# Kernel optimization log

Hardware: AMD Instinct MI355X
Metric: run time of the kernel (lower is better)

Reference implementation:

```python
import jax, jax.numpy as jnp
import numpy as np

B, P, T = 64, 196, 30
E, D, A, ENC, V = 512, 512, 512, 512, 30000


def setup_inputs() -> dict:
    key = jax.random.key(0)
    ks = jax.random.split(key, 24)
    s = 0.02
    return {
        "encoder_feats": jax.random.normal(ks[0], (B, P, ENC), jnp.float32),
        "encoder_pooled": jax.random.normal(ks[1], (B, ENC), jnp.float32),
        "captions": jax.random.randint(ks[2], (B, T), 0, V),
        "We_att": jax.random.normal(ks[3], (ENC, A), jnp.float32) * s,
        "be_att": jnp.zeros((A,), jnp.float32),
        "Wd_att": jax.random.normal(ks[4], (D, A), jnp.float32) * s,
        "bd_att": jnp.zeros((A,), jnp.float32),
        "wf_att": jax.random.normal(ks[5], (A, 1), jnp.float32) * s,
        "bf_att": jnp.zeros((), jnp.float32),
        "emb_table": jax.random.normal(ks[6], (V, E), jnp.float32) * s,
        "W_ih": jax.random.normal(ks[7], (E + ENC, 4 * D), jnp.float32) * s,
        "W_hh": jax.random.normal(ks[8], (D, 4 * D), jnp.float32) * s,
        "b_ih": jnp.zeros((4 * D,), jnp.float32),
        "b_hh": jnp.zeros((4 * D,), jnp.float32),
        "W_init_h": jax.random.normal(ks[9], (ENC, D), jnp.float32) * s,
        "b_init_h": jnp.zeros((D,), jnp.float32),
        "W_init_c": jax.random.normal(ks[10], (ENC, D), jnp.float32) * s,
        "b_init_c": jnp.zeros((D,), jnp.float32),
        "W_fc": jax.random.normal(ks[11], (D, V), jnp.float32) * s,
        "b_fc": jnp.zeros((V,), jnp.float32),
        "W_beta": jax.random.normal(ks[12], (D, ENC), jnp.float32) * s,
        "b_beta": jnp.zeros((ENC,), jnp.float32),
    }


def reference(encoder_feats, encoder_pooled, captions, We_att, be_att, Wd_att,
              bd_att, wf_att, bf_att, emb_table, W_ih, W_hh, b_ih, b_hh,
              W_init_h, b_init_h, W_init_c, b_init_c, W_fc, b_fc, W_beta, b_beta):
    # teacher_forcing_ratio = 1.0, dropout in eval mode (identity)
    emb = emb_table[captions]                              # (B, T, E)
    h = jnp.tanh(encoder_pooled @ W_init_h + b_init_h)     # (B, D)
    c = jnp.tanh(encoder_pooled @ W_init_c + b_init_c)
    enc_proj = encoder_feats @ We_att + be_att             # (B, P, A) precomputed

    def step(carry, emb_t):
        h, c = carry
        dec_proj = h @ Wd_att + bd_att                     # (B, A)
        e = jnp.tanh(enc_proj + dec_proj[:, None, :])      # (B, P, A)
        scores = jnp.squeeze(e @ wf_att, -1) + bf_att      # (B, P)
        alpha = jax.nn.softmax(scores, axis=1)
        ctx = jnp.einsum('bp,bpd->bd', alpha, encoder_feats)
        gate = jax.nn.sigmoid(h @ W_beta + b_beta)
        ctx = gate * ctx
        x = jnp.concatenate([emb_t, ctx], axis=1)          # (B, E+ENC)
        gates = x @ W_ih + b_ih + h @ W_hh + b_hh          # (B, 4D) torch order i,f,g,o
        i, f, g, o = jnp.split(gates, 4, axis=1)
        c2 = jax.nn.sigmoid(f) * c + jax.nn.sigmoid(i) * jnp.tanh(g)
        h2 = jax.nn.sigmoid(o) * jnp.tanh(c2)
        out = h2 @ W_fc + b_fc                             # (B, V)
        return (h2, c2), out

    # inputs at steps t=1..T-1 are teacher-forced embeddings[:, t-1]
    xs = jnp.swapaxes(emb[:, :-1, :], 0, 1)                # (T-1, B, E)
    _, outs = jax.lax.scan(step, (h, c), xs)               # (T-1, B, V)
    outs = jnp.swapaxes(outs, 0, 1)                        # (B, T-1, V)
    zero0 = jnp.zeros((outs.shape[0], 1, outs.shape[2]), outs.dtype)
    return jnp.concatenate([zero0, outs], axis=1)          # (B, T, V)
```

## Files before the change

### kernel.cpp

```cpp
#include <hip/hip_runtime.h>
#include <hip/hip_bf16.h>

#define BB 64
#define PP 196
#define TT 30
#define DD 512
#define VV 30000
#define VPAD 30080
#define MROWS 1856
#define MPAD 1920
#define NBLK 64
#define ASTR 3072
#define ABUF ((size_t)64 * ASTR)

typedef __attribute__((ext_vector_type(8))) short short8;
typedef __attribute__((ext_vector_type(4))) float f32x4;

__device__ __forceinline__ unsigned short f2bf(float f) {
    unsigned int u = __float_as_uint(f);
    unsigned int r = u + 0x7FFFu + ((u >> 16) & 1u);
    return (unsigned short)(r >> 16);
}
__device__ __forceinline__ float bf2f(unsigned short u) {
    return __uint_as_float(((unsigned int)u) << 16);
}
__device__ __forceinline__ float sigf(float x) { return 1.f / (1.f + __expf(-x)); }
__device__ __forceinline__ float tanh_fast(float x) { return 1.f - 2.f / (1.f + __expf(2.f * x)); }
__device__ __forceinline__ unsigned int pack2(unsigned short a, unsigned short b) {
    return (unsigned int)a | ((unsigned int)b << 16);
}
__device__ __forceinline__ void ast_u32(unsigned int* p, unsigned int v) {
    __hip_atomic_store(p, v, __ATOMIC_RELAXED, __HIP_MEMORY_SCOPE_AGENT);
}
__device__ __forceinline__ void ast_f32(float* p, float v) {
    __hip_atomic_store(p, v, __ATOMIC_RELAXED, __HIP_MEMORY_SCOPE_AGENT);
}

__global__ __launch_bounds__(256) void k_cast(const float* __restrict__ in,
                                              unsigned short* __restrict__ out, int n) {
    int i = blockIdx.x * 256 + threadIdx.x;
    int stride = gridDim.x * 256;
    for (; i < n; i += stride) out[i] = f2bf(in[i]);
}

__global__ __launch_bounds__(256) void k_transpose_cast(const float* __restrict__ in,
                                                        unsigned short* __restrict__ out,
                                                        int R, int C, int Cpad, int ostride, int ooff) {
    __shared__ float tile[32][33];
    int tx = threadIdx.x & 31, ty = threadIdx.x >> 5;
    int c0 = blockIdx.x * 32, r0 = blockIdx.y * 32;
#pragma unroll
    for (int i = 0; i < 4; ++i) {
        int r = r0 + ty + i * 8, c = c0 + tx;
        tile[ty + i * 8][tx] = (c < C) ? in[(size_t)r * C + c] : 0.f;
    }
    __syncthreads();
#pragma unroll
    for (int i = 0; i < 4; ++i) {
        int outr = c0 + ty + i * 8, outc = r0 + tx;
        if (outr < Cpad) out[(size_t)outr * ostride + ooff + outc] = f2bf(tile[tx][ty + i * 8]);
    }
}

__global__ __launch_bounds__(256) void k_transpose_cast_split(const float* __restrict__ in,
                                                              unsigned short* __restrict__ out,
                                                              int R, int C, int ostride,
                                                              int ooff, int looff) {
    __shared__ float tile[32][33];
    int tx = threadIdx.x & 31, ty = threadIdx.x >> 5;
    int c0 = blockIdx.x * 32, r0 = blockIdx.y * 32;
#pragma unroll
    for (int i = 0; i < 4; ++i) {
        int r = r0 + ty + i * 8, c = c0 + tx;
        tile[ty + i * 8][tx] = in[(size_t)r * C + c];
    }
    __syncthreads();
#pragma unroll
    for (int i = 0; i < 4; ++i) {
        int outr = c0 + ty + i * 8, outc = r0 + tx;
        float v = tile[tx][ty + i * 8];
        unsigned short hi = f2bf(v);
        unsigned short lo = f2bf(v - bf2f(hi));
        out[(size_t)outr * ostride + ooff + outc] = hi;
        out[(size_t)outr * ostride + looff + outc] = lo;
    }
}

__global__ __launch_bounds__(256) void k_zero0(float* __restrict__ out) {
    int i = blockIdx.x * 256 + threadIdx.x;
    int b = i / VV, v = i - b * VV;
    out[(size_t)b * (TT * VV) + v] = 0.f;
}

__global__ __launch_bounds__(256) void k_init(const float* __restrict__ pooled,
                                              const float* __restrict__ Wh, const float* __restrict__ bh,
                                              const float* __restrict__ Wc, const float* __restrict__ bc,
                                              unsigned short* __restrict__ A1,
                                              float* __restrict__ cbuf, int* __restrict__ bar) {
    int b = blockIdx.x >> 1, which = blockIdx.x & 1, t = threadIdx.x;
    if (blockIdx.x == 0) {
        for (int i = t; i < NBLK * 32 + 32; i += 256) bar[i] = 0;
    }
    const float* W = which ? Wc : Wh;
    const float* bias = which ? bc : bh;
    const float* pr = pooled + b * DD;
    float a0 = 0.f, a1 = 0.f;
#pragma unroll 4
    for (int k = 0; k < DD; ++k) {
        float pv = pr[k];
        a0 += pv * W[k * DD + t];
        a1 += pv * W[k * DD + t + 256];
    }
    float v0 = tanh_fast(a0 + bias[t]);
    float v1 = tanh_fast(a1 + bias[t + 256]);
    if (which == 0) {
        unsigned short hi0 = f2bf(v0), lo0 = f2bf(v0 - bf2f(hi0));
        unsigned short hi1 = f2bf(v1), lo1 = f2bf(v1 - bf2f(hi1));
        unsigned short* xr = A1 + b * ASTR;
        xr[1024 + t] = hi0;        xr[2560 + t] = lo0;
        xr[1024 + t + 256] = hi1;  xr[2560 + t + 256] = lo1;
    } else {
        cbuf[b * DD + t] = v0;
        cbuf[b * DD + t + 256] = v1;
    }
}

__device__ __forceinline__ void gbar(int* bar, int g) {
    __syncthreads();
    asm volatile("s_waitcnt vmcnt(0)" ::: "memory");
    if (threadIdx.x == 0)
        __hip_atomic_store(&bar[blockIdx.x * 32], g, __ATOMIC_RELAXED, __HIP_MEMORY_SCOPE_AGENT);
    if (threadIdx.x < NBLK) {
        while (__hip_atomic_load(&bar[threadIdx.x * 32], __ATOMIC_RELAXED, __HIP_MEMORY_SCOPE_AGENT) < g)
            __builtin_amdgcn_s_sleep(1);
    }
    __syncthreads();
}

#define PA_SUB(S, PH, PL, TILE, NEXT)                                                          \
    ((uint4*)Sa[S])[t] = PH;                                                                   \
    ((uint4*)Sl[S])[t] = PL;                                                                   \
    { int kn = (NEXT) * 32; PH = *(const uint4*)(Ah + kn); PL = *(const uint4*)(Al + kn); }    \
    asm volatile("s_waitcnt lgkmcnt(0)" ::: "memory");                                         \
    __builtin_amdgcn_sched_barrier(0);                                                         \
    __builtin_amdgcn_s_barrier();                                                              \
    __builtin_amdgcn_sched_barrier(0);                                                         \
    { int k0 = (TILE) * 32;                                                                    \
      short8 ah = *(const short8*)&Sa[S][((wave * 16 + r16) * 4 + swz) * 8];                   \
      short8 al = *(const short8*)&Sl[S][((wave * 16 + r16) * 4 + swz) * 8];                   \
      int cu = (k0 >> 3) + kg;                                                                 \
      short8 bh = *(const short8*)&Bp_s[r16 * 1024 + ((cu ^ (r16 & 7)) << 3)];                 \
      short8 bl = *(const short8*)&Bp_s[r16 * 1024 + (((cu + 64) ^ (r16 & 7)) << 3)];          \
      acc = __builtin_amdgcn_mfma_f32_16x16x32_bf16(ah, bh, acc, 0, 0, 0);                     \
      acc = __builtin_amdgcn_mfma_f32_16x16x32_bf16(al, bh, acc, 0, 0, 0);                     \
      acc = __builtin_amdgcn_mfma_f32_16x16x32_bf16(ah, bl, acc, 0, 0, 0); }

#define PC_SUB(S, RAH, RAL, RBH, RBL, TILE, NEXT)                                              \
    ((uint4*)Sa[S])[t] = RAH;  ((uint4*)Sl[S])[t] = RAL;                                       \
    ((uint4*)Sb[S])[t] = RBH;  ((uint4*)Sbl[S])[t] = RBL;                                      \
    { int kn = (NEXT) * 32;                                                                    \
      RAH = *(const uint4*)(Ah + kn); RAL = *(const uint4*)(Al + kn);                          \
      RBH = *(const uint4*)(Bh + kn); RBL = *(const uint4*)(Bl + kn); }                        \
    asm volatile("s_waitcnt lgkmcnt(0)" ::: "memory");                                         \
    __builtin_amdgcn_sched_barrier(0);                                                         \
    __builtin_amdgcn_s_barrier();                                                              \
    __builtin_amdgcn_sched_barrier(0);                                                         \
    { short8 ah = *(const short8*)&Sa[S][((wave * 16 + r16) * 4 + swz) * 8];                   \
      short8 al = *(const short8*)&Sl[S][((wave * 16 + r16) * 4 + swz) * 8];                   \
      _Pragma("unroll")                                                                        \
      for (int g = 0; g < 4; ++g) {                                                            \
          short8 bh = *(const short8*)&Sb[S][((g * 16 + r16) * 4 + swz) * 8];                  \
          short8 bl = *(const short8*)&Sbl[S][((g * 16 + r16) * 4 + swz) * 8];                 \
          acc[g] = __builtin_amdgcn_mfma_f32_16x16x32_bf16(ah, bh, acc[g], 0, 0, 0);           \
          acc[g] = __builtin_amdgcn_mfma_f32_16x16x32_bf16(al, bh, acc[g], 0, 0, 0);           \
          acc[g] = __builtin_amdgcn_mfma_f32_16x16x32_bf16(ah, bl, acc[g], 0, 0, 0);           \
      } }

__global__ __launch_bounds__(256, 1) void k_recur(
    const unsigned short* __restrict__ ep,
    const unsigned short* __restrict__ fb,
    const unsigned short* __restrict__ WdbT,
    const unsigned short* __restrict__ WT,
    const float* __restrict__ bd,
    const float* __restrict__ bbeta,
    const float* __restrict__ wfv,
    const int* __restrict__ caps,
    const float* __restrict__ emb,
    const float* __restrict__ b_ih,
    const float* __restrict__ b_hh,
    unsigned short* __restrict__ A_rot,
    float* __restrict__ cbuf,
    float* __restrict__ dpb_rot,
    unsigned short* __restrict__ hb,
    int* __restrict__ bar) {

    const int blk = blockIdx.x, t = threadIdx.x;
    const int lane = t & 63, wave = t >> 6;
    const int r16 = lane & 15, kg = lane >> 4;
    const int swz = kg ^ ((r16 >> 1) & 3);

    __shared__ unsigned short Bp_s[16 * 1024];
    __shared__ unsigned short Sa[2][2048];
    __shared__ unsigned short Sl[2][2048];
    __shared__ unsigned short Sb[2][2048];
    __shared__ unsigned short Sbl[2][2048];
    __shared__ float sc_s[256];
    __shared__ float red_s[16];
    __shared__ float ctx_s[4][512];

    const int srow = t >> 2, scs = t & 3;
    const int scsrc = scs ^ ((srow >> 1) & 3);

    {
        const unsigned short* src = WdbT + (size_t)(blk * 16) * 1024;
#pragma unroll
        for (int cc = 0; cc < 8; ++cc) {
            int c = t + cc * 256;
            int row = c >> 7, u = c & 127;
            ((uint4*)Bp_s)[row * 128 + (u ^ (row & 7))] =
                *(const uint4*)(src + (size_t)row * 1024 + u * 8);
        }
    }
    __syncthreads();

    int gph = 0;

    for (int ts = 1; ts < TT; ++ts) {
        unsigned short* Acur = A_rot + (size_t)ts * ABUF;
        unsigned short* Anext = Acur + ABUF;
        float* dpb = dpb_rot + (size_t)(ts - 1) * 64 * 1024;

        {
            const int n0 = blk * 16;
            const unsigned short* Ah = Acur + srow * ASTR + 1024 + scsrc * 8;
            const unsigned short* Al = Acur + srow * ASTR + 2560 + scsrc * 8;
            f32x4 acc = {0.f, 0.f, 0.f, 0.f};
            uint4 p0h = *(const uint4*)(Ah + 0),  p0l = *(const uint4*)(Al + 0);
            uint4 p1h = *(const uint4*)(Ah + 32), p1l = *(const uint4*)(Al + 32);
            uint4 p2h = *(const uint4*)(Ah + 64), p2l = *(const uint4*)(Al + 64);
            uint4 p3h = *(const uint4*)(Ah + 96), p3l = *(const uint4*)(Al + 96);
#pragma unroll 1
            for (int i = 0; i < 16; i += 4) {
                PA_SUB(0, p0h, p0l, i + 0, (i + 4 < 16 ? i + 4 : i + 0))
                PA_SUB(1, p1h, p1l, i + 1, (i + 5 < 16 ? i + 5 : i + 1))
                PA_SUB(0, p2h, p2l, i + 2, (i + 6 < 16 ? i + 6 : i + 2))
                PA_SUB(1, p3h, p3l, i + 3, (i + 7 < 16 ? i + 7 : i + 3))
            }
            int col = n0 + r16;
#pragma unroll
            for (int r = 0; r < 4; ++r) {
                int b = wave * 16 + kg * 4 + r;
                float v = acc[r];
                if (col < 512) ast_f32(&dpb[b * 1024 + col], v + bd[col]);
                else ast_f32(&dpb[b * 1024 + col], sigf(v + bbeta[col - 512]));
            }
        }
        gbar(bar, ++gph);

        {
            const int b = blk;
            const int d8 = lane * 8;
            float dsl[8], wsl[8];
            {
                float4 dv0 = *(const float4*)(dpb + b * 1024 + d8);
                float4 dv1 = *(const float4*)(dpb + b * 1024 + d8 + 4);
                float4 wv0 = *(const float4*)(wfv + d8);
                float4 wv1 = *(const float4*)(wfv + d8 + 4);
                dsl[0] = dv0.x; dsl[1] = dv0.y; dsl[2] = dv0.z; dsl[3] = dv0.w;
                dsl[4] = dv1.x; dsl[5] = dv1.y; dsl[6] = dv1.z; dsl[7] = dv1.w;
                wsl[0] = wv0.x; wsl[1] = wv0.y; wsl[2] = wv0.z; wsl[3] = wv0.w;
                wsl[4] = wv1.x; wsl[5] = wv1.y; wsl[6] = wv1.z; wsl[7] = wv1.w;
            }
            const unsigned short* epb = ep + (size_t)(b * PP) * 512;
#pragma unroll 1
            for (int bb = 0; bb < 6; ++bb) {
                uint4 pk[8];
#pragma unroll
                for (int u = 0; u < 8; ++u)
                    pk[u] = *(const uint4*)(epb + (size_t)(wave + 4 * (bb * 8 + u)) * 512 + d8);
#pragma unroll
                for (int u = 0; u < 8; ++u) {
                    const unsigned short* pu = (const unsigned short*)&pk[u];
                    float s = 0.f;
#pragma unroll
                    for (int j = 0; j < 8; ++j)
                        s += tanh_fast(bf2f(pu[j]) + dsl[j]) * wsl[j];
#pragma unroll
                    for (int off = 32; off; off >>= 1) s += __shfl_xor(s, off);
                    if (lane == 0) sc_s[wave + 4 * (bb * 8 + u)] = s;
                }
            }
            {
                uint4 pk = *(const uint4*)(epb + (size_t)(wave + 192) * 512 + d8);
                const unsigned short* pu = (const unsigned short*)&pk;
                float s = 0.f;
#pragma unroll
                for (int j = 0; j < 8; ++j)
                    s += tanh_fast(bf2f(pu[j]) + dsl[j]) * wsl[j];
#pragma unroll
                for (int off = 32; off; off >>= 1) s += __shfl_xor(s, off);
                if (lane == 0) sc_s[wave + 192] = s;
            }
            __syncthreads();
            float sv = (t < PP) ? sc_s[t] : -1e30f;
            float m = sv;
#pragma unroll
            for (int off = 32; off; off >>= 1) m = fmaxf(m, __shfl_xor(m, off));
            if (lane == 0) red_s[wave] = m;
            __syncthreads();
            float mx = fmaxf(fmaxf(red_s[0], red_s[1]), fmaxf(red_s[2], red_s[3]));
            float e = (t < PP) ? __expf(sv - mx) : 0.f;
            float ssum = e;
#pragma unroll
            for (int off = 32; off; off >>= 1) ssum += __shfl_xor(ssum, off);
            if (lane == 0) red_s[8 + wave] = ssum;
            __syncthreads();
            float inv = 1.f / (red_s[8] + red_s[9] + red_s[10] + red_s[11]);
            if (t < PP) sc_s[t] = e * inv;
            __syncthreads();
            const unsigned short* fbb = fb + (size_t)(b * PP) * 512;
            float c[8];
#pragma unroll
            for (int j = 0; j < 8; ++j) c[j] = 0.f;
#pragma unroll 1
            for (int bb = 0; bb < 6; ++bb) {
                uint4 pk[8];
                float av[8];
#pragma unroll
                for (int u = 0; u < 8; ++u) {
                    int p = wave + 4 * (bb * 8 + u);
                    pk[u] = *(const uint4*)(fbb + (size_t)p * 512 + d8);
                    av[u] = sc_s[p];
                }
#pragma unroll
                for (int u = 0; u < 8; ++u) {
                    const unsigned short* pu = (const unsigned short*)&pk[u];
#pragma unroll
                    for (int j = 0; j < 8; ++j) c[j] += av[u] * bf2f(pu[j]);
                }
            }
            {
                int p = wave + 192;
                uint4 pk = *(const uint4*)(fbb + (size_t)p * 512 + d8);
                float a = sc_s[p];
                const unsigned short* pu = (const unsigned short*)&pk;
#pragma unroll
                for (int j = 0; j < 8; ++j) c[j] += a * bf2f(pu[j]);
            }
#pragma unroll
            for (int j = 0; j < 8; ++j) ctx_s[wave][d8 + j] = c[j];
            __syncthreads();
            float2 c0v = *(const float2*)&ctx_s[0][2 * t];
            float2 c1v = *(const float2*)&ctx_s[1][2 * t];
            float2 c2v = *(const float2*)&ctx_s[2][2 * t];
            float2 c3v = *(const float2*)&ctx_s[3][2 * t];
            float ctx0 = c0v.x + c1v.x + c2v.x + c3v.x;
            float ctx1 = c0v.y + c1v.y + c2v.y + c3v.y;
            float2 bt2 = *(const float2*)(dpb + b * 1024 + 512 + 2 * t);
            int tok = caps[b * TT + (ts - 1)];
            const float* er = emb + (size_t)tok * 512;
            float2 ev = *(const float2*)(er + 2 * t);
            unsigned int* xr32 = (unsigned int*)(Acur + (size_t)b * ASTR);
            unsigned short e0h = f2bf(ev.x), e1h = f2bf(ev.y);
            ast_u32(xr32 + t, pack2(e0h, e1h));
            ast_u32(xr32 + 768 + t, pack2(f2bf(ev.x - bf2f(e0h)), f2bf(ev.y - bf2f(e1h))));
            float g0 = bt2.x * ctx0, g1 = bt2.y * ctx1;
            unsigned short g0h = f2bf(g0), g1h = f2bf(g1);
            ast_u32(xr32 + 256 + t, pack2(g0h, g1h));
            ast_u32(xr32 + 1024 + t, pack2(f2bf(g0 - bf2f(g0h)), f2bf(g1 - bf2f(g1h))));
        }
        gbar(bar, ++gph);

        if (blk < 32) {
            const int d0 = blk * 16;
            const unsigned short* Ah = Acur + srow * ASTR + scsrc * 8;
            const unsigned short* Al = Ah + 1536;
            const int jrow = ((srow >> 4) << 9) + d0 + (srow & 15);
            const unsigned short* Bh = WT + (size_t)jrow * 3072 + scsrc * 8;
            const unsigned short* Bl = Bh + 1536;
            f32x4 acc[4];
#pragma unroll
            for (int g = 0; g < 4; ++g) acc[g] = {0.f, 0.f, 0.f, 0.f};
            uint4 a0h = *(const uint4*)(Ah + 0),  a0l = *(const uint4*)(Al + 0);
            uint4 b0h = *(const uint4*)(Bh + 0),  b0l = *(const uint4*)(Bl + 0);
            uint4 a1h = *(const uint4*)(Ah + 32), a1l = *(const uint4*)(Al + 32);
            uint4 b1h = *(const uint4*)(Bh + 32), b1l = *(const uint4*)(Bl + 32);
            uint4 a2h = *(const uint4*)(Ah + 64), a2l = *(const uint4*)(Al + 64);
            uint4 b2h = *(const uint4*)(Bh + 64), b2l = *(const uint4*)(Bl + 64);
            uint4 a3h = *(const uint4*)(Ah + 96), a3l = *(const uint4*)(Al + 96);
            uint4 b3h = *(const uint4*)(Bh + 96), b3l = *(const uint4*)(Bl + 96);
#pragma unroll 1
            for (int i = 0; i < 48; i += 4) {
                PC_SUB(0, a0h, a0l, b0h, b0l, i + 0, (i + 4 < 48 ? i + 4 : i + 0))
                PC_SUB(1, a1h, a1l, b1h, b1l, i + 1, (i + 5 < 48 ? i + 5 : i + 1))
                PC_SUB(0, a2h, a2l, b2h, b2l, i + 2, (i + 6 < 48 ? i + 6 : i + 2))
                PC_SUB(1, a3h, a3l, b3h, b3l, i + 3, (i + 7 < 48 ? i + 7 : i + 3))
            }
            int d = d0 + r16;
            float bi_ = b_ih[d] + b_hh[d];
            float bf_ = b_ih[d + 512] + b_hh[d + 512];
            float bg_ = b_ih[d + 1024] + b_hh[d + 1024];
            float bo_ = b_ih[d + 1536] + b_hh[d + 1536];
#pragma unroll
            for (int r = 0; r < 4; ++r) {
                int b = wave * 16 + kg * 4 + r;
                float gi = sigf(acc[0][r] + bi_);
                float gf = sigf(acc[1][r] + bf_);
                float gg = tanh_fast(acc[2][r] + bg_);
                float go = sigf(acc[3][r] + bo_);
                float cn = gf * cbuf[b * 512 + d] + gi * gg;
                float hn = go * tanh_fast(cn);
                cbuf[b * 512 + d] = cn;
                unsigned short hhi = f2bf(hn);
                unsigned short hlo = f2bf(hn - bf2f(hhi));
                hb[(size_t)((ts - 1) * 64 + b) * 512 + d] = hhi;
                int oh = __shfl_xor((int)hhi, 1);
                int ol = __shfl_xor((int)hlo, 1);
                if ((r16 & 1) == 0) {
                    unsigned int* rw = (unsigned int*)(Anext + (size_t)b * ASTR);
                    ast_u32(rw + 512 + (d >> 1), pack2(hhi, (unsigned short)oh));
                    ast_u32(rw + 1280 + (d >> 1), pack2(hlo, (unsigned short)ol));
                }
            }
        }
        gbar(bar, ++gph);
    }
}

template <int MODE>
__global__ __launch_bounds__(256) void gemm_mfma(const unsigned short* __restrict__ A,
                                                 const unsigned short* __restrict__ Bt,
                                                 const float* __restrict__ bias,
                                                 void* __restrict__ Cv) {
    constexpr int K = 512;
    __shared__ unsigned short As[128 * 32];
    __shared__ unsigned short Bs[128 * 32];
    const int t = threadIdx.x;
    const int m0 = blockIdx.y * 128;
    const int n0 = blockIdx.x * 128;
    const int lane = t & 63, wave = t >> 6;
    const int wm = wave >> 1, wn = wave & 1;
    const int r16 = lane & 15, kg = lane >> 4;
    const int swz = kg ^ ((r16 >> 1) & 3);

    f32x4 acc[4][4];
#pragma unroll
    for (int i = 0; i < 4; ++i)
#pragma unroll
        for (int j = 0; j < 4; ++j) acc[i][j] = {0.f, 0.f, 0.f, 0.f};

    const short8* As8 = (const short8*)As;
    const short8* Bs8 = (const short8*)Bs;

    for (int k0 = 0; k0 < K; k0 += 32) {
#pragma unroll
        for (int i = 0; i < 2; ++i) {
            int u = t + i * 256;
            int row = u >> 2, cs = u & 3;
            int csrc = cs ^ ((row >> 1) & 3);
            ((uint4*)As)[u] = *(const uint4*)(A + (size_t)(m0 + row) * K + k0 + csrc * 8);
            ((uint4*)Bs)[u] = *(const uint4*)(Bt + (size_t)(n0 + row) * K + k0 + csrc * 8);
        }
        __syncthreads();
        short8 af[4], bfr[4];
#pragma unroll
        for (int i = 0; i < 4; ++i) af[i] = As8[(wm * 64 + i * 16 + r16) * 4 + swz];
#pragma unroll
        for (int j = 0; j < 4; ++j) bfr[j] = Bs8[(wn * 64 + j * 16 + r16) * 4 + swz];
#pragma unroll
        for (int i = 0; i < 4; ++i)
#pragma unroll
            for (int j = 0; j < 4; ++j)
                acc[i][j] = __builtin_amdgcn_mfma_f32_16x16x32_bf16(af[i], bfr[j], acc[i][j], 0, 0, 0);
        __syncthreads();
    }

#pragma unroll
    for (int i = 0; i < 4; ++i) {
#pragma unroll
        for (int j = 0; j < 4; ++j) {
            int colg = n0 + wn * 64 + j * 16 + r16;
            float bv;
            if (MODE == 0) bv = bias[colg];
            else bv = (colg < VV) ? bias[colg] : 0.f;
#pragma unroll
            for (int r = 0; r < 4; ++r) {
                int rowg = m0 + wm * 64 + i * 16 + kg * 4 + r;
                float v = acc[i][j][r] + bv;
                if (MODE == 0) {
                    ((unsigned short*)Cv)[(size_t)rowg * 512 + colg] = f2bf(v);
                } else {
                    if (rowg < MROWS && colg < VV) {
                        int tt = rowg >> 6, bb2 = rowg & 63;
                        ((float*)Cv)[(size_t)bb2 * (TT * VV) + (size_t)(tt + 1) * VV + colg] = v;
                    }
                }
            }
        }
    }
}

extern "C" void kernel_launch(void* const* d_in, const int* in_sizes, int n_in,
                              void* d_out, int out_size, void* d_ws, size_t ws_size,
                              hipStream_t stream) {
    const float* feats   = (const float*)d_in[0];
    const float* pooled  = (const float*)d_in[1];
    const int*   caps    = (const int*)d_in[2];
    const float* We      = (const float*)d_in[3];
    const float* be      = (const float*)d_in[4];
    const float* Wd      = (const float*)d_in[5];
    const float* bd      = (const float*)d_in[6];
    const float* wfv     = (const float*)d_in[7];
    const float* emb     = (const float*)d_in[9];
    const float* W_ih    = (const float*)d_in[10];
    const float* W_hh    = (const float*)d_in[11];
    const float* b_ih    = (const float*)d_in[12];
    const float* b_hh    = (const float*)d_in[13];
    const float* W_inh   = (const float*)d_in[14];
    const float* b_inh   = (const float*)d_in[15];
    const float* W_inc   = (const float*)d_in[16];
    const float* b_inc   = (const float*)d_in[17];
    const float* Wfc     = (const float*)d_in[18];
    const float* bfc     = (const float*)d_in[19];
    const float* Wbeta   = (const float*)d_in[20];
    const float* bbeta   = (const float*)d_in[21];
    float* out = (float*)d_out;

    char* ws = (char*)d_ws;
    size_t off = 0;
    auto alloc = [&](size_t bytes) -> char* {
        char* p = ws + off;
        off += (bytes + 255) & ~(size_t)255;
        return p;
    };
    unsigned short* ep_bf = (unsigned short*)alloc((size_t)12544 * 512 * 2);
    unsigned short* fb    = (unsigned short*)alloc((size_t)12544 * 512 * 2);
    unsigned short* WeT   = (unsigned short*)alloc((size_t)512 * 512 * 2);
    unsigned short* WfcT  = (unsigned short*)alloc((size_t)VPAD * 512 * 2);
    unsigned short* WdbT  = (unsigned short*)alloc((size_t)1024 * 1024 * 2);
    unsigned short* WT    = (unsigned short*)alloc((size_t)2048 * 3072 * 2);
    unsigned short* hb    = (unsigned short*)alloc((size_t)MPAD * 512 * 2);
    unsigned short* A_rot = (unsigned short*)alloc((size_t)31 * ABUF * 2);
    float*          dpb   = (float*)alloc((size_t)30 * 64 * 1024 * 4);
    float*          cbuf  = (float*)alloc((size_t)64 * 512 * 4);
    int*            bar   = (int*)alloc((size_t)(NBLK * 32 + 32) * 4);
    (void)ws_size; (void)in_sizes; (void)n_in; (void)out_size;

    k_cast<<<2048, 256, 0, stream>>>(feats, fb, 12544 * 512);
    k_transpose_cast<<<dim3(16, 16), 256, 0, stream>>>(We, WeT, 512, 512, 512, 512, 0);
    k_transpose_cast<<<dim3(940, 16), 256, 0, stream>>>(Wfc, WfcT, 512, VV, VPAD, 512, 0);
    k_transpose_cast_split<<<dim3(16, 16), 256, 0, stream>>>(Wd, WdbT, 512, 512, 1024, 0, 512);
    k_transpose_cast_split<<<dim3(16, 16), 256, 0, stream>>>(Wbeta, WdbT + (size_t)512 * 1024, 512, 512, 1024, 0, 512);
    k_transpose_cast_split<<<dim3(64, 32), 256, 0, stream>>>(W_ih, WT, 1024, 2048, 3072, 0, 1536);
    k_transpose_cast_split<<<dim3(64, 16), 256, 0, stream>>>(W_hh, WT, 512, 2048, 3072, 1024, 2560);
    k_init<<<128, 256, 0, stream>>>(pooled, W_inh, b_inh, W_inc, b_inc, A_rot + ABUF, cbuf, bar);
    gemm_mfma<0><<<dim3(4, 98), 256, 0, stream>>>(fb, WeT, be, ep_bf);
    k_zero0<<<7500, 256, 0, stream>>>(out);

    k_recur<<<NBLK, 256, 0, stream>>>(ep_bf, fb, WdbT, WT, bd, bbeta, wfv, caps, emb,
                                      b_ih, b_hh, A_rot, cbuf, dpb, hb, bar);

    gemm_mfma<1><<<dim3(235, 15), 256, 0, stream>>>(hb, WfcT, bfc, out);
}
```

Before: 2.187 ms.

## Fuse vocab projection into recurrent kernel with consumer blocks overlapping steps

Launches the recurrent kernel with extra consumer blocks that poll a step counter and compute the per-step output projection (h @ W_fc) as soon as each timestep's hidden state is published. This overlaps the large vocab GEMM with the sequential recurrence instead of running it afterwards. It also double-buffers the score and context loads in the attention loop and packs the hb stores into 32-bit writes. It relies on all 256 blocks being co-resident and on the relaxed-atomic flag giving enough ordering, and the consumers may compete with the recurrent blocks for bandwidth.

```diff
diff --git a/kernel.cpp b/kernel.cpp
--- a/kernel.cpp
+++ b/kernel.cpp
@@ -10,6 +10,9 @@
 #define MROWS 1856
 #define MPAD 1920
 #define NBLK 64
+#define NGRID 256
+#define NCONS (NGRID - NBLK)
+#define NTILE 235
 #define ASTR 3072
 #define ABUF ((size_t)64 * ASTR)
 
@@ -176,6 +179,40 @@
           acc[g] = __builtin_amdgcn_mfma_f32_16x16x32_bf16(ah, bl, acc[g], 0, 0, 0);           \
       } }
 
+#define SC_LOAD(PK, BBATCH)                                                                    \
+    _Pragma("unroll")                                                                          \
+    for (int u = 0; u < 8; ++u)                                                                \
+        PK[u] = *(const uint4*)(epb + (size_t)(wave + 4 * ((BBATCH) * 8 + u)) * 512 + d8);
+
+#define SC_COMP(PK, BBATCH)                                                                    \
+    _Pragma("unroll")                                                                          \
+    for (int u = 0; u < 8; ++u) {                                                              \
+        const unsigned short* pu = (const unsigned short*)&PK[u];                              \
+        float s = 0.f;                                                                         \
+        _Pragma("unroll")                                                                      \
+        for (int j = 0; j < 8; ++j)                                                            \
+            s += tanh_fast(bf2f(pu[j]) + dsl[j]) * wsl[j];                                     \
+        _Pragma("unroll")                                                                      \
+        for (int off = 32; off; off >>= 1) s += __shfl_xor(s, off);                            \
+        if (lane == 0) sc_s[wave + 4 * ((BBATCH) * 8 + u)] = s;                                \
+    }
+
+#define CX_LOAD(PK, AV, BBATCH)                                                                \
+    _Pragma("unroll")                                                                          \
+    for (int u = 0; u < 8; ++u) {                                                              \
+        int p = wave + 4 * ((BBATCH) * 8 + u);                                                 \
+        PK[u] = *(const uint4*)(fbb + (size_t)p * 512 + d8);                                   \
+        AV[u] = sc_s[p];                                                                       \
+    }
+
+#define CX_COMP(PK, AV)                                                                        \
+    _Pragma("unroll")                                                                          \
+    for (int u = 0; u < 8; ++u) {                                                              \
+        const unsigned short* pu = (const unsigned short*)&PK[u];                              \
+        _Pragma("unroll")                                                                      \
+        for (int j = 0; j < 8; ++j) c[j] += AV[u] * bf2f(pu[j]);                               \
+    }
+
 __global__ __launch_bounds__(256, 1) void k_recur(
     const unsigned short* __restrict__ ep,
     const unsigned short* __restrict__ fb,
@@ -192,6 +229,9 @@
     float* __restrict__ cbuf,
     float* __restrict__ dpb_rot,
     unsigned short* __restrict__ hb,
+    const unsigned short* __restrict__ WfcT,
+    const float* __restrict__ bfc,
+    float* __restrict__ out,
     int* __restrict__ bar) {
 
     const int blk = blockIdx.x, t = threadIdx.x;
@@ -199,7 +239,7 @@
     const int r16 = lane & 15, kg = lane >> 4;
     const int swz = kg ^ ((r16 >> 1) & 3);
 
-    __shared__ unsigned short Bp_s[16 * 1024];
+    __shared__ unsigned short Bp_s[16 * 1024 + 4096];
     __shared__ unsigned short Sa[2][2048];
     __shared__ unsigned short Sl[2][2048];
     __shared__ unsigned short Sb[2][2048];
@@ -210,6 +250,71 @@
 
     const int srow = t >> 2, scs = t & 3;
     const int scsrc = scs ^ ((srow >> 1) & 3);
+
+    if (blk >= NBLK) {
+        unsigned short* CSa = (unsigned short*)Sa;
+        unsigned short* CSb = (unsigned short*)Sb;
+        const short8* CSa8 = (const short8*)CSa;
+        const short8* CSb8 = (const short8*)CSb;
+        const int cid = blk - NBLK;
+        for (int task = cid; task < 29 * NTILE; task += NCONS) {
+            const int s = task / NTILE;
+            const int ct = task - s * NTILE;
+            if (t == 0) {
+                while (__hip_atomic_load(&bar[NBLK * 32], __ATOMIC_RELAXED, __HIP_MEMORY_SCOPE_AGENT) < s + 1)
+                    __builtin_amdgcn_s_sleep(16);
+            }
+            __syncthreads();
+            const unsigned short* Arow = hb + (size_t)s * 64 * 512;
+            const unsigned short* Brow = WfcT + (size_t)ct * 128 * 512;
+            f32x4 acc[4][2];
+#pragma unroll
+            for (int i = 0; i < 4; ++i) {
+                acc[i][0] = {0.f, 0.f, 0.f, 0.f};
+                acc[i][1] = {0.f, 0.f, 0.f, 0.f};
+            }
+            for (int k0 = 0; k0 < 512; k0 += 32) {
+                {
+                    int row = t >> 2, cs = t & 3, csrc = cs ^ ((row >> 1) & 3);
+                    ((uint4*)CSa)[t] = *(const uint4*)(Arow + (size_t)row * 512 + k0 + csrc * 8);
+                }
+#pragma unroll
+                for (int i2 = 0; i2 < 2; ++i2) {
+                    int u = t + i2 * 256;
+                    int row = u >> 2, cs = u & 3, csrc = cs ^ ((row >> 1) & 3);
+                    ((uint4*)CSb)[u] = *(const uint4*)(Brow + (size_t)row * 512 + k0 + csrc * 8);
+                }
+                __syncthreads();
+                short8 af[4], bfv[2];
+#pragma unroll
+                for (int i = 0; i < 4; ++i) af[i] = CSa8[(i * 16 + r16) * 4 + swz];
+#pragma unroll
+                for (int j = 0; j < 2; ++j) bfv[j] = CSb8[(wave * 32 + j * 16 + r16) * 4 + swz];
+#pragma unroll
+                for (int i = 0; i < 4; ++i)
+#pragma unroll
+                    for (int j = 0; j < 2; ++j)
+                        acc[i][j] = __builtin_amdgcn_mfma_f32_16x16x32_bf16(af[i], bfv[j], acc[i][j], 0, 0, 0);
+                __syncthreads();
+            }
+#pragma unroll
+            for (int j = 0; j < 2; ++j) {
+                int colg = ct * 128 + wave * 32 + j * 16 + r16;
+                float bv = (colg < VV) ? bfc[colg] : 0.f;
+                if (colg < VV) {
+#pragma unroll
+                    for (int i = 0; i < 4; ++i) {
+#pragma unroll
+                        for (int r = 0; r < 4; ++r) {
+                            int b = i * 16 + kg * 4 + r;
+                            out[(size_t)b * (TT * VV) + (size_t)(s + 1) * VV + colg] = acc[i][j][r] + bv;
+                        }
+                    }
+                }
+            }
+        }
+        return;
+    }
 
     {
         const unsigned short* src = WdbT + (size_t)(blk * 16) * 1024;
@@ -272,23 +377,20 @@
                 wsl[4] = wv1.x; wsl[5] = wv1.y; wsl[6] = wv1.z; wsl[7] = wv1.w;
             }
             const unsigned short* epb = ep + (size_t)(b * PP) * 512;
-#pragma unroll 1
-            for (int bb = 0; bb < 6; ++bb) {
-                uint4 pk[8];
-#pragma unroll
-                for (int u = 0; u < 8; ++u)
-                    pk[u] = *(const uint4*)(epb + (size_t)(wave + 4 * (bb * 8 + u)) * 512 + d8);
-#pragma unroll
-                for (int u = 0; u < 8; ++u) {
-                    const unsigned short* pu = (const unsigned short*)&pk[u];
-                    float s = 0.f;
-#pragma unroll
-                    for (int j = 0; j < 8; ++j)
-                        s += tanh_fast(bf2f(pu[j]) + dsl[j]) * wsl[j];
-#pragma unroll
-                    for (int off = 32; off; off >>= 1) s += __shfl_xor(s, off);
-                    if (lane == 0) sc_s[wave + 4 * (bb * 8 + u)] = s;
-                }
+            {
+                uint4 pkA[8], pkB[8];
+                SC_LOAD(pkA, 0)
+                SC_LOAD(pkB, 1)
+                SC_COMP(pkA, 0)
+                SC_LOAD(pkA, 2)
+                SC_COMP(pkB, 1)
+                SC_LOAD(pkB, 3)
+                SC_COMP(pkA, 2)
+                SC_LOAD(pkA, 4)
+                SC_COMP(pkB, 3)
+                SC_LOAD(pkB, 5)
+                SC_COMP(pkA, 4)
+                SC_COMP(pkB, 5)
             }
             {
                 uint4 pk = *(const uint4*)(epb + (size_t)(wave + 192) * 512 + d8);
@@ -322,22 +424,21 @@
             float c[8];
 #pragma unroll
             for (int j = 0; j < 8; ++j) c[j] = 0.f;
-#pragma unroll 1
-            for (int bb = 0; bb < 6; ++bb) {
-                uint4 pk[8];
-                float av[8];
-#pragma unroll
-                for (int u = 0; u < 8; ++u) {
-                    int p = wave + 4 * (bb * 8 + u);
-                    pk[u] = *(const uint4*)(fbb + (size_t)p * 512 + d8);
-                    av[u] = sc_s[p];
-                }
-#pragma unroll
-                for (int u = 0; u < 8; ++u) {
-                    const unsigned short* pu = (const unsigned short*)&pk[u];
-#pragma unroll
-                    for (int j = 0; j < 8; ++j) c[j] += av[u] * bf2f(pu[j]);
-                }
+            {
+                uint4 qkA[8], qkB[8];
+                float avA[8], avB[8];
+                CX_LOAD(qkA, avA, 0)
+                CX_LOAD(qkB, avB, 1)
+                CX_COMP(qkA, avA)
+                CX_LOAD(qkA, avA, 2)
+                CX_COMP(qkB, avB)
+                CX_LOAD(qkB, avB, 3)
+                CX_COMP(qkA, avA)
+                CX_LOAD(qkA, avA, 4)
+                CX_COMP(qkB, avB)
+                CX_LOAD(qkB, avB, 5)
+                CX_COMP(qkA, avA)
+                CX_COMP(qkB, avB)
             }
             {
                 int p = wave + 192;
@@ -413,25 +514,27 @@
                 cbuf[b * 512 + d] = cn;
                 unsigned short hhi = f2bf(hn);
                 unsigned short hlo = f2bf(hn - bf2f(hhi));
-                hb[(size_t)((ts - 1) * 64 + b) * 512 + d] = hhi;
                 int oh = __shfl_xor((int)hhi, 1);
                 int ol = __shfl_xor((int)hlo, 1);
                 if ((r16 & 1) == 0) {
                     unsigned int* rw = (unsigned int*)(Anext + (size_t)b * ASTR);
                     ast_u32(rw + 512 + (d >> 1), pack2(hhi, (unsigned short)oh));
                     ast_u32(rw + 1280 + (d >> 1), pack2(hlo, (unsigned short)ol));
+                    ast_u32((unsigned int*)hb + ((size_t)((ts - 1) * 64 + b)) * 256 + (d >> 1),
+                            pack2(hhi, (unsigned short)oh));
                 }
             }
         }
         gbar(bar, ++gph);
-    }
-}
-
-template <int MODE>
-__global__ __launch_bounds__(256) void gemm_mfma(const unsigned short* __restrict__ A,
-                                                 const unsigned short* __restrict__ Bt,
-                                                 const float* __restrict__ bias,
-                                                 void* __restrict__ Cv) {
+        if (blk == 0 && t == 0)
+            __hip_atomic_store(&bar[NBLK * 32], ts, __ATOMIC_RELAXED, __HIP_MEMORY_SCOPE_AGENT);
+    }
+}
+
+__global__ __launch_bounds__(256) void gemm_mfma0(const unsigned short* __restrict__ A,
+                                                  const unsigned short* __restrict__ Bt,
+                                                  const float* __restrict__ bias,
+                                                  unsigned short* __restrict__ Cv) {
     constexpr int K = 512;
     __shared__ unsigned short As[128 * 32];
     __shared__ unsigned short Bs[128 * 32];
@@ -480,21 +583,11 @@
 #pragma unroll
         for (int j = 0; j < 4; ++j) {
             int colg = n0 + wn * 64 + j * 16 + r16;
-            float bv;
-            if (MODE == 0) bv = bias[colg];
-            else bv = (colg < VV) ? bias[colg] : 0.f;
+            float bv = bias[colg];
 #pragma unroll
             for (int r = 0; r < 4; ++r) {
                 int rowg = m0 + wm * 64 + i * 16 + kg * 4 + r;
-                float v = acc[i][j][r] + bv;
-                if (MODE == 0) {
-                    ((unsigned short*)Cv)[(size_t)rowg * 512 + colg] = f2bf(v);
-                } else {
-                    if (rowg < MROWS && colg < VV) {
-                        int tt = rowg >> 6, bb2 = rowg & 63;
-                        ((float*)Cv)[(size_t)bb2 * (TT * VV) + (size_t)(tt + 1) * VV + colg] = v;
-                    }
-                }
+                Cv[(size_t)rowg * 512 + colg] = f2bf(acc[i][j][r] + bv);
             }
         }
     }
@@ -554,11 +647,9 @@
     k_transpose_cast_split<<<dim3(64, 32), 256, 0, stream>>>(W_ih, WT, 1024, 2048, 3072, 0, 1536);
     k_transpose_cast_split<<<dim3(64, 16), 256, 0, stream>>>(W_hh, WT, 512, 2048, 3072, 1024, 2560);
     k_init<<<128, 256, 0, stream>>>(pooled, W_inh, b_inh, W_inc, b_inc, A_rot + ABUF, cbuf, bar);
-    gemm_mfma<0><<<dim3(4, 98), 256, 0, stream>>>(fb, WeT, be, ep_bf);
+    gemm_mfma0<<<dim3(4, 98), 256, 0, stream>>>(fb, WeT, be, ep_bf);
     k_zero0<<<7500, 256, 0, stream>>>(out);
 
-    k_recur<<<NBLK, 256, 0, stream>>>(ep_bf, fb, WdbT, WT, bd, bbeta, wfv, caps, emb,
-                                      b_ih, b_hh, A_rot, cbuf, dpb, hb, bar);
-
-    gemm_mfma<1><<<dim3(235, 15), 256, 0, stream>>>(hb, WfcT, bfc, out);
-}
+    k_recur<<<NGRID, 256, 0, stream>>>(ep_bf, fb, WdbT, WT, bd, bbeta, wfv, caps, emb,
+                                       b_ih, b_hh, A_rot, cbuf, dpb, hb, WfcT, bfc, out, bar);
+}
```

After: 2.216 ms. About the same (+1.3%).
